# Optimization experiments

Hardware: AMD Instinct MI355X
Metric: run time of the kernel (lower is better)

## Reference

```python
import jax, jax.numpy as jnp
import numpy as np

N, K, C = 128, 64, 64

def _w(key, shape, scale):
    return (jax.random.normal(key, shape, dtype=jnp.float32) * scale)

def setup_inputs() -> dict:
    key = jax.random.key(0)
    ks = jax.random.split(key, 20)
    s1 = 1.0 / np.sqrt(C)
    s2 = 1.0 / np.sqrt(2 * C)
    inp = {
        "x": jax.random.normal(ks[0], (N, K, C), dtype=jnp.float32),
        "W_lin": _w(ks[1], (C, C), s1), "b_lin": jnp.zeros((C,), jnp.float32),
        # unary_passing: Linear(C,C) -> tanh -> Linear(C,C)
        "Wu1": _w(ks[2], (C, C), s1), "bu1": jnp.zeros((C,), jnp.float32),
        "Wu2": _w(ks[3], (C, C), s1), "bu2": jnp.zeros((C,), jnp.float32),
        # unary_gate: Linear(C,C) -> tanh -> Linear(C,C) -> sigmoid
        "Wug1": _w(ks[4], (C, C), s1), "bug1": jnp.zeros((C,), jnp.float32),
        "Wug2": _w(ks[5], (C, C), s1), "bug2": jnp.zeros((C,), jnp.float32),
        # binary_passing: Linear(2C,C) -> tanh -> Linear(C,C)
        "Wb1": _w(ks[6], (2 * C, C), s2), "bb1": jnp.zeros((C,), jnp.float32),
        "Wb2": _w(ks[7], (C, C), s1), "bb2": jnp.zeros((C,), jnp.float32),
        # binary_gate: Linear(2C,C) -> tanh -> Linear(C,C) -> sigmoid
        "Wbg1": _w(ks[8], (2 * C, C), s2), "bbg1": jnp.zeros((C,), jnp.float32),
        "Wbg2": _w(ks[9], (C, C), s1), "bbg2": jnp.zeros((C,), jnp.float32),
        "t": 0,  # time scalar, ignored by IgnoreLinear base layer
    }
    return inp


def reference(x, W_lin, b_lin, Wu1, bu1, Wu2, bu2, Wug1, bug1, Wug2, bug2,
              Wb1, bb1, Wb2, bb2, Wbg1, bbg1, Wbg2, bbg2, t):
    # base linear map (IgnoreLinear: ignores t)
    h = x @ W_lin + b_lin                          # (N, K, C)
    n, k, c = h.shape
    # unary message with gate
    um = jnp.tanh(h @ Wu1 + bu1) @ Wu2 + bu2
    ug = jax.nn.sigmoid(jnp.tanh(h @ Wug1 + bug1) @ Wug2 + bug2)
    um = um * ug                                   # (N, K, C)
    # all-pairs broadcast-concat: hm[n,i,j] = [h[n,j], h[n,i]]
    hm = jnp.concatenate([
        jnp.broadcast_to(h[:, None, :, :], (n, k, k, c)),
        jnp.broadcast_to(h[:, :, None, :], (n, k, k, c)),
    ], axis=3)                                     # (N, K, K, 2C)
    bm = jnp.tanh(hm @ Wb1 + bb1) @ Wb2 + bb2      # (N, K, K, C)
    bg = jax.nn.sigmoid(jnp.tanh(hm @ Wbg1 + bbg1) @ Wbg2 + bbg2)
    # sum over axis 1 (includes diagonal, as in original), normalize by K-1
    bm = jnp.sum(bm * bg, axis=1) / jnp.float32(k - 1)  # (N, K, C)
    return um + bm
```

## Files before the change

kernel.cpp:

```cpp
#include <hip/hip_runtime.h>

#define WST 72

typedef __attribute__((ext_vector_type(4))) float    f32x4;
typedef __attribute__((ext_vector_type(2))) float    f32x2;
typedef __attribute__((ext_vector_type(8))) _Float16 f16x8;
typedef __attribute__((ext_vector_type(2))) _Float16 f16x2;

__device__ __forceinline__ float rcp_f(float x) { return __builtin_amdgcn_rcpf(x); }
__device__ __forceinline__ float fast_sigmoid(float x) {
    return rcp_f(1.0f + __expf(-x));
}
__device__ __forceinline__ float tanh_exp(float x) {
    return 1.0f - 2.0f * rcp_f(__expf(2.0f * x) + 1.0f);
}

__device__ __forceinline__ void stage512(const float* __restrict__ W,
                                         _Float16* Wt, int tid) {
#pragma unroll
    for (int i = 0; i < 8; ++i) {
        int idx = tid + i * 512;
        int k = idx >> 6, c = idx & 63;
        Wt[c * WST + k] = (_Float16)W[idx];
    }
}

__device__ __forceinline__ void gemm2(const _Float16* Act, int arow, int qd,
                                      const _Float16* Wt, int colb,
                                      f32x4 acc[2]) {
    f16x8 a0 = *(const f16x8*)(Act + arow * WST + qd * 8);
    f16x8 a1 = *(const f16x8*)(Act + arow * WST + 32 + qd * 8);
#pragma unroll
    for (int cc = 0; cc < 2; ++cc) {
        const _Float16* wr = Wt + (colb + cc * 16) * WST + qd * 8;
        f16x8 b0 = *(const f16x8*)(wr);
        f16x8 b1 = *(const f16x8*)(wr + 32);
        acc[cc] = __builtin_amdgcn_mfma_f32_16x16x32_f16(a0, b0, acc[cc], 0, 0, 0);
        acc[cc] = __builtin_amdgcn_mfma_f32_16x16x32_f16(a1, b1, acc[cc], 0, 0, 0);
    }
}

__global__ __launch_bounds__(512, 2) void fused_all_kernel(
    const float* __restrict__ x,
    const float* __restrict__ W_lin, const float* __restrict__ b_lin,
    const float* __restrict__ Wu1,  const float* __restrict__ bu1,
    const float* __restrict__ Wu2,  const float* __restrict__ bu2,
    const float* __restrict__ Wug1, const float* __restrict__ bug1,
    const float* __restrict__ Wug2, const float* __restrict__ bug2,
    const float* __restrict__ Wb1,  const float* __restrict__ bb1,
    const float* __restrict__ Wb2,  const float* __restrict__ bb2,
    const float* __restrict__ Wbg1, const float* __restrict__ bbg1,
    const float* __restrict__ Wbg2, const float* __restrict__ bbg2,
    float* __restrict__ out)
{
    __shared__ __align__(16) char smem[113664];
    _Float16* Wt0  = (_Float16*)(smem);
    _Float16* Wt1  = (_Float16*)(smem + 9216);
    _Float16* Ax   = (_Float16*)(smem + 18432);
    _Float16* Ah   = (_Float16*)(smem + 27648);
    _Float16* Au   = (_Float16*)(smem + 36864);
    _Float16* Agg  = (_Float16*)(smem + 46080);
    float*    EQb  = (float*)(smem + 55296);
    float*    EQgb = (float*)(smem + 71680);
    float*    EPm  = (float*)(smem + 88064);
    float*    EPgm = (float*)(smem + 96768);
    float*    um32 = (float*)(smem + 105472);
    float*    Red  = (float*)(smem);

    int tid = threadIdx.x, w = tid >> 6, l = tid & 63;
    int qd = l >> 4, l16 = l & 15;
    int n = blockIdx.x >> 1, jsel = blockIdx.x & 1;

    int rw = w & 3, ch = w >> 2;
    int arow = rw * 16 + l16;
    int colb = ch * 32 + l16;
    int crow = rw * 16 + qd * 4;
    bool mine = (rw >> 1) == jsel;
    int lr0 = (rw & 1) * 16 + qd * 4;

    f32x4 acc[2];

#pragma unroll
    for (int i = 0; i < 4; ++i) {
        int e = tid * 2 + i * 1024;
        f32x2 v = *(const f32x2*)(x + (size_t)n * 4096 + e);
        f16x2 p; p[0] = (_Float16)v[0]; p[1] = (_Float16)v[1];
        *(f16x2*)(Ax + (e >> 6) * WST + (e & 63)) = p;
    }
    stage512(W_lin, Wt0, tid);
    __syncthreads();

#pragma unroll
    for (int cc = 0; cc < 2; ++cc) {
        float bv = b_lin[colb + cc * 16];
        acc[cc] = (f32x4){bv, bv, bv, bv};
    }
    gemm2(Ax, arow, qd, Wt0, colb, acc);
#pragma unroll
    for (int cc = 0; cc < 2; ++cc)
#pragma unroll
        for (int r = 0; r < 4; ++r)
            Ah[(crow + r) * WST + colb + cc * 16] = (_Float16)acc[cc][r];
    stage512(Wb1, Wt1, tid);
    __syncthreads();

#pragma unroll
    for (int cc = 0; cc < 2; ++cc) {
        float bv = bb1[colb + cc * 16];
        acc[cc] = (f32x4){bv, bv, bv, bv};
    }
    gemm2(Ah, arow, qd, Wt1, colb, acc);
    if (mine) {
#pragma unroll
        for (int cc = 0; cc < 2; ++cc)
#pragma unroll
            for (int r = 0; r < 4; ++r)
                EPm[(lr0 + r) * 68 + colb + cc * 16] = __expf(2.0f * acc[cc][r]);
    }
    stage512(Wb1 + 4096, Wt0, tid);
    __syncthreads();

    acc[0] = (f32x4){0.f, 0.f, 0.f, 0.f};
    acc[1] = (f32x4){0.f, 0.f, 0.f, 0.f};
    gemm2(Ah, arow, qd, Wt0, colb, acc);
#pragma unroll
    for (int cc = 0; cc < 2; ++cc)
#pragma unroll
        for (int r = 0; r < 4; ++r)
            EQb[(crow + r) * 64 + colb + cc * 16] = __expf(2.0f * acc[cc][r]);
    stage512(Wbg1, Wt1, tid);
    __syncthreads();

#pragma unroll
    for (int cc = 0; cc < 2; ++cc) {
        float bv = bbg1[colb + cc * 16];
        acc[cc] = (f32x4){bv, bv, bv, bv};
    }
    gemm2(Ah, arow, qd, Wt1, colb, acc);
    if (mine) {
#pragma unroll
        for (int cc = 0; cc < 2; ++cc)
#pragma unroll
            for (int r = 0; r < 4; ++r)
                EPgm[(lr0 + r) * 68 + colb + cc * 16] = __expf(2.0f * acc[cc][r]);
    }
    stage512(Wbg1 + 4096, Wt0, tid);
    __syncthreads();

    acc[0] = (f32x4){0.f, 0.f, 0.f, 0.f};
    acc[1] = (f32x4){0.f, 0.f, 0.f, 0.f};
    gemm2(Ah, arow, qd, Wt0, colb, acc);
#pragma unroll
    for (int cc = 0; cc < 2; ++cc)
#pragma unroll
        for (int r = 0; r < 4; ++r)
            EQgb[(crow + r) * 64 + colb + cc * 16] = __expf(2.0f * acc[cc][r]);
    stage512(Wu1, Wt1, tid);
    __syncthreads();

#pragma unroll
    for (int cc = 0; cc < 2; ++cc) {
        float bv = bu1[colb + cc * 16];
        acc[cc] = (f32x4){bv, bv, bv, bv};
    }
    gemm2(Ah, arow, qd, Wt1, colb, acc);
#pragma unroll
    for (int cc = 0; cc < 2; ++cc)
#pragma unroll
        for (int r = 0; r < 4; ++r)
            Au[(crow + r) * WST + colb + cc * 16] = (_Float16)tanh_exp(acc[cc][r]);
    stage512(Wug1, Wt0, tid);
    __syncthreads();

#pragma unroll
    for (int cc = 0; cc < 2; ++cc) {
        float bv = bug1[colb + cc * 16];
        acc[cc] = (f32x4){bv, bv, bv, bv};
    }
    gemm2(Ah, arow, qd, Wt0, colb, acc);
#pragma unroll
    for (int cc = 0; cc < 2; ++cc)
#pragma unroll
        for (int r = 0; r < 4; ++r)
            Agg[(crow + r) * WST + colb + cc * 16] = (_Float16)tanh_exp(acc[cc][r]);
    stage512(Wu2, Wt1, tid);
    __syncthreads();

    f32x4 uacc[2];
#pragma unroll
    for (int cc = 0; cc < 2; ++cc) {
        float bv = bu2[colb + cc * 16];
        uacc[cc] = (f32x4){bv, bv, bv, bv};
    }
    gemm2(Au, arow, qd, Wt1, colb, uacc);
    stage512(Wug2, Wt0, tid);
    __syncthreads();

#pragma unroll
    for (int cc = 0; cc < 2; ++cc) {
        float bv = bug2[colb + cc * 16];
        acc[cc] = (f32x4){bv, bv, bv, bv};
    }
    gemm2(Agg, arow, qd, Wt0, colb, acc);
    if (mine) {
#pragma unroll
        for (int cc = 0; cc < 2; ++cc)
#pragma unroll
            for (int r = 0; r < 4; ++r)
                um32[(lr0 + r) * 64 + colb + cc * 16] =
                    uacc[cc][r] * fast_sigmoid(acc[cc][r]);
    }
    stage512(Wb2, Wt1, tid);
    stage512(Wbg2, Au, tid);
    __syncthreads();

    int jgrp = w >> 2, iw = w & 3;

    f16x8 bwm[4][2], bwg[4][2];
#pragma unroll
    for (int cc = 0; cc < 4; ++cc)
#pragma unroll
        for (int kk = 0; kk < 2; ++kk) {
            bwm[cc][kk] = *(const f16x8*)(Wt1 + (cc * 16 + l16) * WST + kk * 32 + qd * 8);
            bwg[cc][kk] = *(const f16x8*)(Au  + (cc * 16 + l16) * WST + kk * 32 + qd * 8);
        }
    float bim[4], big[4];
#pragma unroll
    for (int cc = 0; cc < 4; ++cc) {
        bim[cc] = bb2[cc * 16 + l16];
        big[cc] = bbg2[cc * 16 + l16];
    }

    const float* pr  = EPm  + (jgrp * 16 + l16) * 68;
    const float* pgr = EPgm + (jgrp * 16 + l16) * 68;
    f32x4 pm[4], pg[4];
    pm[0] = *(const f32x4*)(pr + qd * 8);
    pm[1] = *(const f32x4*)(pr + qd * 8 + 4);
    pm[2] = *(const f32x4*)(pr + 32 + qd * 8);
    pm[3] = *(const f32x4*)(pr + 32 + qd * 8 + 4);
    pg[0] = *(const f32x4*)(pgr + qd * 8);
    pg[1] = *(const f32x4*)(pgr + qd * 8 + 4);
    pg[2] = *(const f32x4*)(pgr + 32 + qd * 8);
    pg[3] = *(const f32x4*)(pgr + 32 + qd * 8 + 4);

    f32x4 bacc[4];
#pragma unroll
    for (int cc = 0; cc < 4; ++cc) bacc[cc] = (f32x4){0.f, 0.f, 0.f, 0.f};

    for (int ii = iw * 16; ii < iw * 16 + 16; ++ii) {
        const float* qm = EQb  + ii * 64;
        const float* qg = EQgb + ii * 64;
        f16x8 am[2], ag[2];
#pragma unroll
        for (int kk = 0; kk < 2; ++kk) {
            int cb = kk * 32 + qd * 8;
            f32x4 qa = *(const f32x4*)(qm + cb);
            f32x4 qb = *(const f32x4*)(qm + cb + 4);
            f32x4 ha = *(const f32x4*)(qg + cb);
            f32x4 hb = *(const f32x4*)(qg + cb + 4);
#pragma unroll
            for (int t = 0; t < 4; ++t) {
                am[kk][t]     = (_Float16)(1.0f - 2.0f * rcp_f(__builtin_fmaf(pm[kk*2][t],   qa[t], 1.0f)));
                am[kk][t + 4] = (_Float16)(1.0f - 2.0f * rcp_f(__builtin_fmaf(pm[kk*2+1][t], qb[t], 1.0f)));
                ag[kk][t]     = (_Float16)(1.0f - 2.0f * rcp_f(__builtin_fmaf(pg[kk*2][t],   ha[t], 1.0f)));
                ag[kk][t + 4] = (_Float16)(1.0f - 2.0f * rcp_f(__builtin_fmaf(pg[kk*2+1][t], hb[t], 1.0f)));
            }
        }
#pragma unroll
        for (int cc = 0; cc < 4; ++cc) {
            f32x4 d = {bim[cc], bim[cc], bim[cc], bim[cc]};
            d = __builtin_amdgcn_mfma_f32_16x16x32_f16(am[0], bwm[cc][0], d, 0, 0, 0);
            d = __builtin_amdgcn_mfma_f32_16x16x32_f16(am[1], bwm[cc][1], d, 0, 0, 0);
            f32x4 e = {big[cc], big[cc], big[cc], big[cc]};
            e = __builtin_amdgcn_mfma_f32_16x16x32_f16(ag[0], bwg[cc][0], e, 0, 0, 0);
            e = __builtin_amdgcn_mfma_f32_16x16x32_f16(ag[1], bwg[cc][1], e, 0, 0, 0);
#pragma unroll
            for (int r = 0; r < 4; ++r)
                bacc[cc][r] += d[r] * fast_sigmoid(e[r]);
        }
    }

    __syncthreads();
#pragma unroll
    for (int cc = 0; cc < 4; ++cc)
#pragma unroll
        for (int r = 0; r < 4; ++r)
            Red[(jgrp * 4 + iw) * 1024 + (qd * 4 + r) * 64 + cc * 16 + l16] = bacc[cc][r];
    __syncthreads();

    {
        int e = tid * 4;
        int lr = e >> 6, col = e & 63;
        int g = lr >> 4, rr = lr & 15;
        f32x4 s = {0.f, 0.f, 0.f, 0.f};
#pragma unroll
        for (int w2 = 0; w2 < 4; ++w2)
            s += *(const f32x4*)(Red + (g * 4 + w2) * 1024 + rr * 64 + col);
        f32x4 u = *(const f32x4*)(um32 + lr * 64 + col);
        f32x4 o;
#pragma unroll
        for (int t = 0; t < 4; ++t)
            o[t] = u[t] + s[t] * (1.0f / 63.0f);
        *(f32x4*)(out + (size_t)n * 4096 + (size_t)(jsel * 32 + lr) * 64 + col) = o;
    }
}

extern "C" void kernel_launch(void* const* d_in, const int* in_sizes, int n_in,
                              void* d_out, int out_size, void* d_ws, size_t ws_size,
                              hipStream_t stream)
{
    (void)in_sizes; (void)n_in; (void)out_size; (void)d_ws; (void)ws_size;
    const float* x     = (const float*)d_in[0];
    const float* W_lin = (const float*)d_in[1];
    const float* b_lin = (const float*)d_in[2];
    const float* Wu1   = (const float*)d_in[3];
    const float* bu1   = (const float*)d_in[4];
    const float* Wu2   = (const float*)d_in[5];
    const float* bu2   = (const float*)d_in[6];
    const float* Wug1  = (const float*)d_in[7];
    const float* bug1  = (const float*)d_in[8];
    const float* Wug2  = (const float*)d_in[9];
    const float* bug2  = (const float*)d_in[10];
    const float* Wb1   = (const float*)d_in[11];
    const float* bb1   = (const float*)d_in[12];
    const float* Wb2   = (const float*)d_in[13];
    const float* bb2   = (const float*)d_in[14];
    const float* Wbg1  = (const float*)d_in[15];
    const float* bbg1  = (const float*)d_in[16];
    const float* Wbg2  = (const float*)d_in[17];
    const float* bbg2  = (const float*)d_in[18];

    hipLaunchKernelGGL(fused_all_kernel, dim3(256), dim3(512), 0, stream,
        x, W_lin, b_lin, Wu1, bu1, Wu2, bu2, Wug1, bug1, Wug2, bug2,
        Wb1, bb1, Wb2, bb2, Wbg1, bbg1, Wbg2, bbg2,
        (float*)d_out);
}
```

Before: 118.7 us.

## Restructure prologue GEMMs across wave groups and fold tanh affine into weights

The prologue is reorganized so two wave groups compute different projections concurrently. Only the rows each block needs are computed, and the next weights are prefetched into registers before the current GEMM. The inner pairwise loop now uses the identity tanh = 1 - 2/(1+e) with the -2 scale folded into the second-layer weights and column sums folded into the bias, so each element needs only a reciprocal. Pairs of elements share one reciprocal (1/(ab)), and values are packed with cvt_pkrtz, cutting transcendental and conversion instructions in the hot loop. The trade-offs are some precision risk from the shared reciprocal and round-toward-zero conversion, plus extra shared-memory aliasing.

New measurement: 117.2 us. Within noise of the previous version (-1.3%).

```diff
diff --git a/kernel.cpp b/kernel.cpp
--- a/kernel.cpp
+++ b/kernel.cpp
@@ -6,6 +6,9 @@
 typedef __attribute__((ext_vector_type(2))) float    f32x2;
 typedef __attribute__((ext_vector_type(8))) _Float16 f16x8;
 typedef __attribute__((ext_vector_type(2))) _Float16 f16x2;
+typedef __attribute__((ext_vector_type(2))) __fp16   fp16x2_raw;
+
+union U8 { f16x8 v; f16x2 h[4]; };
 
 __device__ __forceinline__ float rcp_f(float x) { return __builtin_amdgcn_rcpf(x); }
 __device__ __forceinline__ float fast_sigmoid(float x) {
@@ -14,14 +17,31 @@
 __device__ __forceinline__ float tanh_exp(float x) {
     return 1.0f - 2.0f * rcp_f(__expf(2.0f * x) + 1.0f);
 }
-
-__device__ __forceinline__ void stage512(const float* __restrict__ W,
-                                         _Float16* Wt, int tid) {
+__device__ __forceinline__ f16x2 pkrtz(float a, float b) {
+    fp16x2_raw r = __builtin_amdgcn_cvt_pkrtz(a, b);
+    return __builtin_bit_cast(f16x2, r);
+}
+
+__device__ __forceinline__ void wload8(const float* __restrict__ W, int tid, float v[8]) {
+#pragma unroll
+    for (int i = 0; i < 8; ++i) v[i] = W[tid + i * 512];
+}
+__device__ __forceinline__ void wstore8(_Float16* Wt, int tid, const float v[8], float scale) {
 #pragma unroll
     for (int i = 0; i < 8; ++i) {
         int idx = tid + i * 512;
-        int k = idx >> 6, c = idx & 63;
-        Wt[c * WST + k] = (_Float16)W[idx];
+        Wt[(idx & 63) * WST + (idx >> 6)] = (_Float16)(v[i] * scale);
+    }
+}
+__device__ __forceinline__ void wload16(const float* __restrict__ W, int t256, float v[16]) {
+#pragma unroll
+    for (int i = 0; i < 16; ++i) v[i] = W[t256 + i * 256];
+}
+__device__ __forceinline__ void wstore16(_Float16* Wt, int t256, const float v[16]) {
+#pragma unroll
+    for (int i = 0; i < 16; ++i) {
+        int idx = t256 + i * 256;
+        Wt[(idx & 63) * WST + (idx >> 6)] = (_Float16)v[i];
     }
 }
 
@@ -57,7 +77,11 @@
     _Float16* Wt0  = (_Float16*)(smem);
     _Float16* Wt1  = (_Float16*)(smem + 9216);
     _Float16* Ax   = (_Float16*)(smem + 18432);
+    _Float16* Tu   = (_Float16*)(smem + 18432);
+    _Float16* Tg   = (_Float16*)(smem + 23040);
     _Float16* Ah   = (_Float16*)(smem + 27648);
+    float*    csum_m = (float*)(smem + 27648);
+    float*    csum_g = (float*)(smem + 27904);
     _Float16* Au   = (_Float16*)(smem + 36864);
     _Float16* Agg  = (_Float16*)(smem + 46080);
     float*    EQb  = (float*)(smem + 55296);
@@ -75,10 +99,13 @@
     int arow = rw * 16 + l16;
     int colb = ch * 32 + l16;
     int crow = rw * 16 + qd * 4;
-    bool mine = (rw >> 1) == jsel;
-    int lr0 = (rw & 1) * 16 + qd * 4;
-
-    f32x4 acc[2];
+
+    bool gA = (w < 4);
+    int w2 = w & 3;
+    int t256 = tid & 255;
+    int lr16 = (w2 & 1) * 16;
+    int cb32 = (w2 >> 1) * 32;
+    int arow32 = jsel * 32 + lr16 + l16;
 
 #pragma unroll
     for (int i = 0; i < 4; ++i) {
@@ -87,131 +114,175 @@
         f16x2 p; p[0] = (_Float16)v[0]; p[1] = (_Float16)v[1];
         *(f16x2*)(Ax + (e >> 6) * WST + (e & 63)) = p;
     }
-    stage512(W_lin, Wt0, tid);
-    __syncthreads();
-
-#pragma unroll
-    for (int cc = 0; cc < 2; ++cc) {
-        float bv = b_lin[colb + cc * 16];
-        acc[cc] = (f32x4){bv, bv, bv, bv};
-    }
-    gemm2(Ax, arow, qd, Wt0, colb, acc);
-#pragma unroll
-    for (int cc = 0; cc < 2; ++cc)
+    {
+        float wv[8];
+        wload8(W_lin, tid, wv);
+        wstore8(Wt0, tid, wv, 1.0f);
+    }
+    __syncthreads();
+
+    {
+        float wv[16];
+        wload16(gA ? Wb1 : Wb1 + 4096, t256, wv);
+        f32x4 acc[2];
+#pragma unroll
+        for (int cc = 0; cc < 2; ++cc) {
+            float bv = b_lin[colb + cc * 16];
+            acc[cc] = (f32x4){bv, bv, bv, bv};
+        }
+        gemm2(Ax, arow, qd, Wt0, colb, acc);
+#pragma unroll
+        for (int cc = 0; cc < 2; ++cc)
+#pragma unroll
+            for (int r = 0; r < 4; ++r)
+                Ah[(crow + r) * WST + colb + cc * 16] = (_Float16)acc[cc][r];
+        wstore16(gA ? Wt1 : Au, t256, wv);
+    }
+    __syncthreads();
+
+    {
+        float wv[16];
+        wload16(gA ? Wbg1 : Wbg1 + 4096, t256, wv);
+        if (gA) {
+            f32x4 acc[2];
+#pragma unroll
+            for (int cc = 0; cc < 2; ++cc) {
+                float bv = bb1[cb32 + cc * 16 + l16];
+                acc[cc] = (f32x4){bv, bv, bv, bv};
+            }
+            gemm2(Ah, arow32, qd, Wt1, cb32 + l16, acc);
+#pragma unroll
+            for (int cc = 0; cc < 2; ++cc)
+#pragma unroll
+                for (int r = 0; r < 4; ++r)
+                    EPm[(lr16 + qd * 4 + r) * 68 + cb32 + cc * 16 + l16] =
+                        __expf(2.0f * acc[cc][r]);
+            wstore16(Ax, t256, wv);
+        } else {
+            f32x4 a4[2][2];
+#pragma unroll
+            for (int hh = 0; hh < 2; ++hh) {
+                a4[hh][0] = (f32x4){0.f, 0.f, 0.f, 0.f};
+                a4[hh][1] = (f32x4){0.f, 0.f, 0.f, 0.f};
+            }
+            gemm2(Ah, w2 * 16 + l16, qd, Au, l16, a4[0]);
+            gemm2(Ah, w2 * 16 + l16, qd, Au, 32 + l16, a4[1]);
+#pragma unroll
+            for (int hh = 0; hh < 2; ++hh)
+#pragma unroll
+                for (int cc = 0; cc < 2; ++cc)
+#pragma unroll
+                    for (int r = 0; r < 4; ++r)
+                        EQb[(w2 * 16 + qd * 4 + r) * 64 + hh * 32 + cc * 16 + l16] =
+                            __expf(2.0f * a4[hh][cc][r]);
+            wstore16(Wt0, t256, wv);
+        }
+    }
+    __syncthreads();
+
+    {
+        float wv[16];
+        wload16(gA ? Wu1 : Wug1, t256, wv);
+        if (gA) {
+            f32x4 acc[2];
+#pragma unroll
+            for (int cc = 0; cc < 2; ++cc) {
+                float bv = bbg1[cb32 + cc * 16 + l16];
+                acc[cc] = (f32x4){bv, bv, bv, bv};
+            }
+            gemm2(Ah, arow32, qd, Ax, cb32 + l16, acc);
+#pragma unroll
+            for (int cc = 0; cc < 2; ++cc)
+#pragma unroll
+                for (int r = 0; r < 4; ++r)
+                    EPgm[(lr16 + qd * 4 + r) * 68 + cb32 + cc * 16 + l16] =
+                        __expf(2.0f * acc[cc][r]);
+            wstore16(Wt1, t256, wv);
+        } else {
+            f32x4 a4[2][2];
+#pragma unroll
+            for (int hh = 0; hh < 2; ++hh) {
+                a4[hh][0] = (f32x4){0.f, 0.f, 0.f, 0.f};
+                a4[hh][1] = (f32x4){0.f, 0.f, 0.f, 0.f};
+            }
+            gemm2(Ah, w2 * 16 + l16, qd, Wt0, l16, a4[0]);
+            gemm2(Ah, w2 * 16 + l16, qd, Wt0, 32 + l16, a4[1]);
+#pragma unroll
+            for (int hh = 0; hh < 2; ++hh)
+#pragma unroll
+                for (int cc = 0; cc < 2; ++cc)
+#pragma unroll
+                    for (int r = 0; r < 4; ++r)
+                        EQgb[(w2 * 16 + qd * 4 + r) * 64 + hh * 32 + cc * 16 + l16] =
+                            __expf(2.0f * a4[hh][cc][r]);
+            wstore16(Au, t256, wv);
+        }
+    }
+    __syncthreads();
+
+    {
+        float wv[16];
+        wload16(gA ? Wu2 : Wug2, t256, wv);
+        const _Float16* Bw = gA ? Wt1 : Au;
+        const float* bias1 = gA ? bu1 : bug1;
+        _Float16* Tdst = gA ? Tu : Tg;
+        f32x4 acc[2];
+#pragma unroll
+        for (int cc = 0; cc < 2; ++cc) {
+            float bv = bias1[cb32 + cc * 16 + l16];
+            acc[cc] = (f32x4){bv, bv, bv, bv};
+        }
+        gemm2(Ah, arow32, qd, Bw, cb32 + l16, acc);
+#pragma unroll
+        for (int cc = 0; cc < 2; ++cc)
+#pragma unroll
+            for (int r = 0; r < 4; ++r)
+                Tdst[(lr16 + qd * 4 + r) * WST + cb32 + cc * 16 + l16] =
+                    (_Float16)tanh_exp(acc[cc][r]);
+        wstore16(gA ? Agg : Wt0, t256, wv);
+    }
+    __syncthreads();
+
+    {
+        float wm[8], wg2[8];
+        wload8(Wb2, tid, wm);
+        wload8(Wbg2, tid, wg2);
+        float cs = 0.0f;
+        bool docs = (w < 2);
+        if (docs) {
+            const float* Wp = (w == 0) ? Wb2 : Wbg2;
+            int c = tid & 63;
+#pragma unroll
+            for (int k = 0; k < 64; ++k)
+                cs += (float)(_Float16)Wp[k * 64 + c];
+            cs += ((w == 0) ? bb2 : bbg2)[c];
+        }
+        int rw5 = w & 1, ch5 = w >> 1;
+        int ar5 = (rw5 * 16 + l16) * WST;
+        int c5 = ch5 * 16 + l16;
+        f16x8 a0 = *(const f16x8*)(Tu + ar5 + qd * 8);
+        f16x8 a1 = *(const f16x8*)(Tu + ar5 + 32 + qd * 8);
+        f16x8 b0 = *(const f16x8*)(Agg + c5 * WST + qd * 8);
+        f16x8 b1 = *(const f16x8*)(Agg + c5 * WST + 32 + qd * 8);
+        float bv = bu2[c5];
+        f32x4 ua = (f32x4){bv, bv, bv, bv};
+        ua = __builtin_amdgcn_mfma_f32_16x16x32_f16(a0, b0, ua, 0, 0, 0);
+        ua = __builtin_amdgcn_mfma_f32_16x16x32_f16(a1, b1, ua, 0, 0, 0);
+        a0 = *(const f16x8*)(Tg + ar5 + qd * 8);
+        a1 = *(const f16x8*)(Tg + ar5 + 32 + qd * 8);
+        b0 = *(const f16x8*)(Wt0 + c5 * WST + qd * 8);
+        b1 = *(const f16x8*)(Wt0 + c5 * WST + 32 + qd * 8);
+        bv = bug2[c5];
+        f32x4 ga = (f32x4){bv, bv, bv, bv};
+        ga = __builtin_amdgcn_mfma_f32_16x16x32_f16(a0, b0, ga, 0, 0, 0);
+        ga = __builtin_amdgcn_mfma_f32_16x16x32_f16(a1, b1, ga, 0, 0, 0);
 #pragma unroll
         for (int r = 0; r < 4; ++r)
-            Ah[(crow + r) * WST + colb + cc * 16] = (_Float16)acc[cc][r];
-    stage512(Wb1, Wt1, tid);
-    __syncthreads();
-
-#pragma unroll
-    for (int cc = 0; cc < 2; ++cc) {
-        float bv = bb1[colb + cc * 16];
-        acc[cc] = (f32x4){bv, bv, bv, bv};
-    }
-    gemm2(Ah, arow, qd, Wt1, colb, acc);
-    if (mine) {
-#pragma unroll
-        for (int cc = 0; cc < 2; ++cc)
-#pragma unroll
-            for (int r = 0; r < 4; ++r)
-                EPm[(lr0 + r) * 68 + colb + cc * 16] = __expf(2.0f * acc[cc][r]);
-    }
-    stage512(Wb1 + 4096, Wt0, tid);
-    __syncthreads();
-
-    acc[0] = (f32x4){0.f, 0.f, 0.f, 0.f};
-    acc[1] = (f32x4){0.f, 0.f, 0.f, 0.f};
-    gemm2(Ah, arow, qd, Wt0, colb, acc);
-#pragma unroll
-    for (int cc = 0; cc < 2; ++cc)
-#pragma unroll
-        for (int r = 0; r < 4; ++r)
-            EQb[(crow + r) * 64 + colb + cc * 16] = __expf(2.0f * acc[cc][r]);
-    stage512(Wbg1, Wt1, tid);
-    __syncthreads();
-
-#pragma unroll
-    for (int cc = 0; cc < 2; ++cc) {
-        float bv = bbg1[colb + cc * 16];
-        acc[cc] = (f32x4){bv, bv, bv, bv};
-    }
-    gemm2(Ah, arow, qd, Wt1, colb, acc);
-    if (mine) {
-#pragma unroll
-        for (int cc = 0; cc < 2; ++cc)
-#pragma unroll
-            for (int r = 0; r < 4; ++r)
-                EPgm[(lr0 + r) * 68 + colb + cc * 16] = __expf(2.0f * acc[cc][r]);
-    }
-    stage512(Wbg1 + 4096, Wt0, tid);
-    __syncthreads();
-
-    acc[0] = (f32x4){0.f, 0.f, 0.f, 0.f};
-    acc[1] = (f32x4){0.f, 0.f, 0.f, 0.f};
-    gemm2(Ah, arow, qd, Wt0, colb, acc);
-#pragma unroll
-    for (int cc = 0; cc < 2; ++cc)
-#pragma unroll
-        for (int r = 0; r < 4; ++r)
-            EQgb[(crow + r) * 64 + colb + cc * 16] = __expf(2.0f * acc[cc][r]);
-    stage512(Wu1, Wt1, tid);
-    __syncthreads();
-
-#pragma unroll
-    for (int cc = 0; cc < 2; ++cc) {
-        float bv = bu1[colb + cc * 16];
-        acc[cc] = (f32x4){bv, bv, bv, bv};
-    }
-    gemm2(Ah, arow, qd, Wt1, colb, acc);
-#pragma unroll
-    for (int cc = 0; cc < 2; ++cc)
-#pragma unroll
-        for (int r = 0; r < 4; ++r)
-            Au[(crow + r) * WST + colb + cc * 16] = (_Float16)tanh_exp(acc[cc][r]);
-    stage512(Wug1, Wt0, tid);
-    __syncthreads();
-
-#pragma unroll
-    for (int cc = 0; cc < 2; ++cc) {
-        float bv = bug1[colb + cc * 16];
-        acc[cc] = (f32x4){bv, bv, bv, bv};
-    }
-    gemm2(Ah, arow, qd, Wt0, colb, acc);
-#pragma unroll
-    for (int cc = 0; cc < 2; ++cc)
-#pragma unroll
-        for (int r = 0; r < 4; ++r)
-            Agg[(crow + r) * WST + colb + cc * 16] = (_Float16)tanh_exp(acc[cc][r]);
-    stage512(Wu2, Wt1, tid);
-    __syncthreads();
-
-    f32x4 uacc[2];
-#pragma unroll
-    for (int cc = 0; cc < 2; ++cc) {
-        float bv = bu2[colb + cc * 16];
-        uacc[cc] = (f32x4){bv, bv, bv, bv};
-    }
-    gemm2(Au, arow, qd, Wt1, colb, uacc);
-    stage512(Wug2, Wt0, tid);
-    __syncthreads();
-
-#pragma unroll
-    for (int cc = 0; cc < 2; ++cc) {
-        float bv = bug2[colb + cc * 16];
-        acc[cc] = (f32x4){bv, bv, bv, bv};
-    }
-    gemm2(Agg, arow, qd, Wt0, colb, acc);
-    if (mine) {
-#pragma unroll
-        for (int cc = 0; cc < 2; ++cc)
-#pragma unroll
-            for (int r = 0; r < 4; ++r)
-                um32[(lr0 + r) * 64 + colb + cc * 16] =
-                    uacc[cc][r] * fast_sigmoid(acc[cc][r]);
-    }
-    stage512(Wb2, Wt1, tid);
-    stage512(Wbg2, Au, tid);
+            um32[(rw5 * 16 + qd * 4 + r) * 64 + c5] = ua[r] * fast_sigmoid(ga[r]);
+        wstore8(Wt1, tid, wm, -2.0f);
+        wstore8(Au, tid, wg2, -2.0f);
+        if (docs) ((w == 0) ? csum_m : csum_g)[tid & 63] = cs;
+    }
     __syncthreads();
 
     int jgrp = w >> 2, iw = w & 3;
@@ -227,8 +298,8 @@
     float bim[4], big[4];
 #pragma unroll
     for (int cc = 0; cc < 4; ++cc) {
-        bim[cc] = bb2[cc * 16 + l16];
-        big[cc] = bbg2[cc * 16 + l16];
+        bim[cc] = csum_m[cc * 16 + l16];
+        big[cc] = csum_g[cc * 16 + l16];
     }
 
     const float* pr  = EPm  + (jgrp * 16 + l16) * 68;
@@ -250,7 +321,7 @@
     for (int ii = iw * 16; ii < iw * 16 + 16; ++ii) {
         const float* qm = EQb  + ii * 64;
         const float* qg = EQgb + ii * 64;
-        f16x8 am[2], ag[2];
+        U8 am[2], ag[2];
 #pragma unroll
         for (int kk = 0; kk < 2; ++kk) {
             int cb = kk * 32 + qd * 8;
@@ -259,21 +330,33 @@
             f32x4 ha = *(const f32x4*)(qg + cb);
             f32x4 hb = *(const f32x4*)(qg + cb + 4);
 #pragma unroll
-            for (int t = 0; t < 4; ++t) {
-                am[kk][t]     = (_Float16)(1.0f - 2.0f * rcp_f(__builtin_fmaf(pm[kk*2][t],   qa[t], 1.0f)));
-                am[kk][t + 4] = (_Float16)(1.0f - 2.0f * rcp_f(__builtin_fmaf(pm[kk*2+1][t], qb[t], 1.0f)));
-                ag[kk][t]     = (_Float16)(1.0f - 2.0f * rcp_f(__builtin_fmaf(pg[kk*2][t],   ha[t], 1.0f)));
-                ag[kk][t + 4] = (_Float16)(1.0f - 2.0f * rcp_f(__builtin_fmaf(pg[kk*2+1][t], hb[t], 1.0f)));
+            for (int t = 0; t < 2; ++t) {
+                float a0 = __builtin_fmaf(pm[kk*2][2*t],   qa[2*t],   1.0f);
+                float a1 = __builtin_fmaf(pm[kk*2][2*t+1], qa[2*t+1], 1.0f);
+                float ri = rcp_f(a0 * a1);
+                am[kk].h[t]     = pkrtz(ri * a1, ri * a0);
+                float b0f = __builtin_fmaf(pm[kk*2+1][2*t],   qb[2*t],   1.0f);
+                float b1f = __builtin_fmaf(pm[kk*2+1][2*t+1], qb[2*t+1], 1.0f);
+                float rj = rcp_f(b0f * b1f);
+                am[kk].h[2 + t] = pkrtz(rj * b1f, rj * b0f);
+                float c0 = __builtin_fmaf(pg[kk*2][2*t],   ha[2*t],   1.0f);
+                float c1 = __builtin_fmaf(pg[kk*2][2*t+1], ha[2*t+1], 1.0f);
+                float rk = rcp_f(c0 * c1);
+                ag[kk].h[t]     = pkrtz(rk * c1, rk * c0);
+                float d0 = __builtin_fmaf(pg[kk*2+1][2*t],   hb[2*t],   1.0f);
+                float d1 = __builtin_fmaf(pg[kk*2+1][2*t+1], hb[2*t+1], 1.0f);
+                float rl = rcp_f(d0 * d1);
+                ag[kk].h[2 + t] = pkrtz(rl * d1, rl * d0);
             }
         }
 #pragma unroll
         for (int cc = 0; cc < 4; ++cc) {
             f32x4 d = {bim[cc], bim[cc], bim[cc], bim[cc]};
-            d = __builtin_amdgcn_mfma_f32_16x16x32_f16(am[0], bwm[cc][0], d, 0, 0, 0);
-            d = __builtin_amdgcn_mfma_f32_16x16x32_f16(am[1], bwm[cc][1], d, 0, 0, 0);
+            d = __builtin_amdgcn_mfma_f32_16x16x32_f16(am[0].v, bwm[cc][0], d, 0, 0, 0);
+            d = __builtin_amdgcn_mfma_f32_16x16x32_f16(am[1].v, bwm[cc][1], d, 0, 0, 0);
             f32x4 e = {big[cc], big[cc], big[cc], big[cc]};
-            e = __builtin_amdgcn_mfma_f32_16x16x32_f16(ag[0], bwg[cc][0], e, 0, 0, 0);
-            e = __builtin_amdgcn_mfma_f32_16x16x32_f16(ag[1], bwg[cc][1], e, 0, 0, 0);
+            e = __builtin_amdgcn_mfma_f32_16x16x32_f16(ag[0].v, bwg[cc][0], e, 0, 0, 0);
+            e = __builtin_amdgcn_mfma_f32_16x16x32_f16(ag[1].v, bwg[cc][1], e, 0, 0, 0);
 #pragma unroll
             for (int r = 0; r < 4; ++r)
                 bacc[cc][r] += d[r] * fast_sigmoid(e[r]);
@@ -294,8 +377,8 @@
         int g = lr >> 4, rr = lr & 15;
         f32x4 s = {0.f, 0.f, 0.f, 0.f};
 #pragma unroll
-        for (int w2 = 0; w2 < 4; ++w2)
-            s += *(const f32x4*)(Red + (g * 4 + w2) * 1024 + rr * 64 + col);
+        for (int w2r = 0; w2r < 4; ++w2r)
+            s += *(const f32x4*)(Red + (g * 4 + w2r) * 1024 + rr * 64 + col);
         f32x4 u = *(const f32x4*)(um32 + lr * 64 + col);
         f32x4 o;
 #pragma unroll
```
